# Performance work log

Hardware: AMD Instinct MI355X
Metric: run time of the kernel (lower is better)

Reference implementation:

```python
import jax, jax.numpy as jnp
import numpy as np

N_NODES = 50000
N_EDGES = 1600000
IN_DIM = 256
OUT_DIM = 32
N_HEADS = 4
ALPHA = 0.2


def setup_inputs() -> dict:
    key = jax.random.key(0)
    k1, k2, k3, k4 = jax.random.split(key, 4)
    h = jax.random.normal(k1, (N_NODES, IN_DIM), dtype=jnp.float32)
    adj_indices = jax.random.randint(k2, (2, N_EDGES), 0, N_NODES, dtype=jnp.int32)
    # xavier_uniform with gain=1.414 (matching torch init scale)
    def xavier(k, shape, gain=1.414):
        fan_in, fan_out = shape[0], shape[1]
        lim = gain * np.sqrt(6.0 / (fan_in + fan_out))
        return jax.random.uniform(k, shape, jnp.float32, -lim, lim)
    W = xavier(k3, (IN_DIM, OUT_DIM * N_HEADS))
    a = xavier(k4, (2 * OUT_DIM, N_HEADS))
    return {"h": h, "adj_indices": adj_indices, "W": W, "a": a}


def reference(h, adj_indices, W, a):
    N = h.shape[0]
    # project: [N, H, D]
    h_prime = (h @ W).reshape(N, N_HEADS, OUT_DIM)
    src = adj_indices[0]
    dst = adj_indices[1]
    h_src = h_prime[src]  # [E, H, D]
    h_dst = h_prime[dst]  # [E, H, D]
    a_src = a[:OUT_DIM]   # [D, H]
    a_dst = a[OUT_DIM:]   # [D, H]
    # attention logits per edge, per head: [E, H]
    att = jnp.einsum('ehd,dh->eh', h_src, a_src) + jnp.einsum('ehd,dh->eh', h_dst, a_dst)
    att = jax.nn.leaky_relu(att, negative_slope=ALPHA)
    # scatter-softmax over destination nodes (stable)
    m = jax.ops.segment_max(att, dst, num_segments=N)          # [N, H]
    e = jnp.exp(att - m[dst])                                   # [E, H]
    s = jax.ops.segment_sum(e, dst, num_segments=N)             # [N, H]
    att_norm = e / s[dst]                                       # [E, H]
    # weighted scatter-add aggregation: [N, H, D]
    agg = jax.ops.segment_sum(att_norm[:, :, None] * h_src, dst, num_segments=N)
    out = agg.reshape(N, N_HEADS * OUT_DIM)
    # dropout=0.0 (eval / identity)
    return out
```

## Files before the change

### kernel.cpp

```cpp
#include <hip/hip_runtime.h>

#define N_NODES 50000
#define N_EDGES 1600000
#define IN_DIM  256
#define OUT_D   128
#define NEG_SLOPE 0.2f
#define NBIN 256
#define BINW 196
#define CAP  8192
#define KDUP 8
#define NPW  25
#define SCAP 1536

typedef unsigned short ushort_t;
typedef short bf16x8 __attribute__((ext_vector_type(8)));
typedef float f32x4 __attribute__((ext_vector_type(4)));

__device__ __forceinline__ ushort_t f2bf(float f) {
    unsigned u = __float_as_uint(f);
    u = (u + 0x7FFF + ((u >> 16) & 1)) >> 16;
    return (ushort_t)u;
}

__global__ __launch_bounds__(256) void wprep_kernel(const float* __restrict__ W,
                                                    ushort_t* __restrict__ wt) {
    int i0 = (blockIdx.x * 256 + threadIdx.x) * 4;
    f32x4 v = *(const f32x4*)(W + i0);
    int k = i0 >> 7;
    int n0 = i0 & 127;
    int byte_in_row = 2 * k;
#pragma unroll
    for (int j = 0; j < 4; ++j) {
        int n = n0 + j;
        int sw = ((byte_in_row & ~15) ^ ((n & 7) << 4)) | (byte_in_row & 15);
        wt[(n << 8) + (sw >> 1)] = f2bf(v[j]);
    }
}

__global__ __launch_bounds__(256) void gemm_kernel(const float* __restrict__ h,
                                                   const ushort_t* __restrict__ wt,
                                                   const float* __restrict__ a,
                                                   ushort_t* __restrict__ hp,
                                                   float* __restrict__ asrc,
                                                   float* __restrict__ adst) {
    __shared__ ushort_t sW[32768];
    int t = threadIdx.x;
    for (int i = t * 8; i < 32768; i += 2048)
        *(bf16x8*)(sW + i) = *(const bf16x8*)(wt + i);
    __syncthreads();

    int wave = t >> 6, lane = t & 63;
    int l15 = lane & 15, quad = lane >> 4;
    int rowbase = blockIdx.x * 128 + wave * 16;

    f32x4 acc[2][8] = {};
#pragma unroll
    for (int ks = 0; ks < 8; ++ks) {
        bf16x8 af[2];
#pragma unroll
        for (int rt = 0; rt < 2; ++rt) {
            int arow = rowbase + rt * 64 + l15;
            if (arow >= N_NODES) arow = N_NODES - 1;
            const float* ap = h + (size_t)arow * IN_DIM + quad * 8 + ks * 32;
            f32x4 lo = *(const f32x4*)ap;
            f32x4 hi = *(const f32x4*)(ap + 4);
#pragma unroll
            for (int j = 0; j < 4; ++j) {
                af[rt][j]     = (short)f2bf(lo[j]);
                af[rt][4 + j] = (short)f2bf(hi[j]);
            }
        }
        int koff = ks * 64 + quad * 16;
#pragma unroll
        for (int tn = 0; tn < 8; ++tn) {
            int n = tn * 16 + l15;
            int swz = koff ^ ((n & 7) << 4);
            bf16x8 bfr = *(const bf16x8*)((const char*)sW + n * 512 + swz);
            acc[0][tn] = __builtin_amdgcn_mfma_f32_16x16x32_bf16(af[0], bfr, acc[0][tn], 0, 0, 0);
            acc[1][tn] = __builtin_amdgcn_mfma_f32_16x16x32_bf16(af[1], bfr, acc[1][tn], 0, 0, 0);
        }
    }

    float aS[8], aD[8];
#pragma unroll
    for (int tn = 0; tn < 8; ++tn) {
        int col = tn * 16 + l15;
        int dd = col & 31, hh = col >> 5;
        aS[tn] = a[dd * 4 + hh];
        aD[tn] = a[(32 + dd) * 4 + hh];
    }

#pragma unroll
    for (int rt = 0; rt < 2; ++rt)
#pragma unroll
        for (int r = 0; r < 4; ++r) {
            int row = rowbase + rt * 64 + quad * 4 + r;
            float pS[4] = {0.f, 0.f, 0.f, 0.f}, pD[4] = {0.f, 0.f, 0.f, 0.f};
#pragma unroll
            for (int tn = 0; tn < 8; ++tn) {
                float v = acc[rt][tn][r];
                pS[tn >> 1] += v * aS[tn];
                pD[tn >> 1] += v * aD[tn];
            }
#pragma unroll
            for (int o = 1; o < 16; o <<= 1) {
#pragma unroll
                for (int hh = 0; hh < 4; ++hh) {
                    pS[hh] += __shfl_xor(pS[hh], o, 16);
                    pD[hh] += __shfl_xor(pD[hh], o, 16);
                }
            }
            if (row < N_NODES) {
                if (l15 == 0) { f32x4 v = {pS[0], pS[1], pS[2], pS[3]}; *(f32x4*)(asrc + row * 4) = v; }
                if (l15 == 1) { f32x4 v = {pD[0], pD[1], pD[2], pD[3]}; *(f32x4*)(adst + row * 4) = v; }
            }
        }

#pragma unroll
    for (int rt = 0; rt < 2; ++rt)
#pragma unroll
        for (int tn = 0; tn < 8; ++tn) {
            int col = tn * 16 + l15;
#pragma unroll
            for (int r = 0; r < 4; ++r) {
                int row = rowbase + rt * 64 + quad * 4 + r;
                if (row < N_NODES) hp[(size_t)row * OUT_D + col] = f2bf(acc[rt][tn][r]);
            }
        }
}

__global__ __launch_bounds__(256) void binA_kernel(const int* __restrict__ src,
                                                   const int* __restrict__ dst,
                                                   int* __restrict__ tail,
                                                   unsigned* __restrict__ binbuf) {
    __shared__ unsigned stage[8192];
    __shared__ int cnt[256], lcnt[256], lbase[256], gbase[256], sc[256];
    int t = threadIdx.x;
    cnt[t] = 0; lcnt[t] = 0;
    __syncthreads();

    int blockbase = blockIdx.x * 8192;
    int n = min(8192, N_EDGES - blockbase);
    int e0 = blockbase + t * 32;
    int d[32], s[32];
#pragma unroll
    for (int q = 0; q < 8; ++q) {
        if (t * 32 + q * 4 + 4 <= n) {
            int4 dv = *(const int4*)(dst + e0 + q * 4);
            int4 sv = *(const int4*)(src + e0 + q * 4);
            d[q*4+0]=dv.x; d[q*4+1]=dv.y; d[q*4+2]=dv.z; d[q*4+3]=dv.w;
            s[q*4+0]=sv.x; s[q*4+1]=sv.y; s[q*4+2]=sv.z; s[q*4+3]=sv.w;
        } else {
#pragma unroll
            for (int r = 0; r < 4; ++r) {
                int g = t * 32 + q * 4 + r;
                d[q*4+r] = (g < n) ? dst[e0 + q*4 + r] : -1;
                s[q*4+r] = (g < n) ? src[e0 + q*4 + r] : 0;
            }
        }
    }
#pragma unroll
    for (int j = 0; j < 32; ++j)
        if (d[j] >= 0) atomicAdd(&cnt[(unsigned)d[j] / BINW], 1);
    __syncthreads();
    gbase[t] = atomicAdd(&tail[t], cnt[t]);
    sc[t] = cnt[t]; __syncthreads();
#pragma unroll
    for (int off = 1; off < 256; off <<= 1) {
        int v = (t >= off) ? sc[t - off] : 0;
        __syncthreads();
        sc[t] += v;
        __syncthreads();
    }
    lbase[t] = sc[t] - cnt[t];
    __syncthreads();
#pragma unroll
    for (int j = 0; j < 32; ++j) {
        if (d[j] >= 0) {
            unsigned p = (unsigned)d[j] / BINW;
            unsigned ldst = (unsigned)d[j] - p * BINW;
            int pos = lbase[p] + atomicAdd(&lcnt[p], 1);
            stage[pos] = (unsigned)s[j] | (ldst << 16) | (p << 24);
        }
    }
    __syncthreads();
    for (int i = t; i < n; i += 256) {
        unsigned v = stage[i];
        unsigned p = v >> 24;
        int pos = gbase[p] + (i - lbase[p]);
        if (pos < CAP) binbuf[(size_t)p * CAP + pos] = v & 0xFFFFFFu;
    }
}

__global__ __launch_bounds__(256) void aggB_kernel(const unsigned* __restrict__ binbuf,
                                                   const int* __restrict__ tail,
                                                   const float* __restrict__ asrc,
                                                   const float* __restrict__ adst,
                                                   const ushort_t* __restrict__ hp,
                                                   float* __restrict__ out) {
    int b = blockIdx.x >> 3, j = blockIdx.x & 7;
    __shared__ ushort_t lcsr[SCAP];
    __shared__ int cnt[32], sc[32], excl[32], lcur[32];
    __shared__ int   s_i[4][64];
    __shared__ f32x4 s_p[4][64];
    int t = threadIdx.x;
    int count = min(tail[b], CAP);
    const unsigned* buf = binbuf + (size_t)b * CAP;
    int lo = j * NPW;
    int hi = min(lo + NPW, BINW);

    if (t < 32) cnt[t] = 0;
    __syncthreads();
    for (int i = t; i < count; i += 256) {
        int ld = (buf[i] >> 16) & 0xFF;
        if (ld >= lo && ld < hi) atomicAdd(&cnt[ld - lo], 1);
    }
    __syncthreads();
    if (t < 64) {
        int v = (t < 32) ? cnt[t] : 0;
#pragma unroll
        for (int off = 1; off < 32; off <<= 1) {
            int u = __shfl_up(v, off, 64);
            if (t >= off) v += u;
        }
        if (t < 32) { sc[t] = v; excl[t] = v - cnt[t]; lcur[t] = v - cnt[t]; }
    }
    __syncthreads();
    for (int i = t; i < count; i += 256) {
        unsigned v = buf[i];
        int ld = (v >> 16) & 0xFF;
        if (ld >= lo && ld < hi) {
            int pos = atomicAdd(&lcur[ld - lo], 1);
            if (pos < SCAP) lcsr[pos] = (ushort_t)(v & 0xFFFF);
        }
    }
    __syncthreads();

    int wave = t >> 6, lane = t & 63;
    int l15 = lane & 15, grp = lane >> 4;
    int hd = l15 >> 2;

    for (int ld = lo + wave; ld < hi; ld += 4) {
        int d = b * BINW + ld;
        if (d >= N_NODES) continue;
        int s0 = min(excl[ld - lo], SCAP), s1 = min(sc[ld - lo], SCAP);
        f32x4 ad = *(const f32x4*)(adst + d * 4);
        float sum[4] = {0.f, 0.f, 0.f, 0.f};
        f32x4 accA = {0.f, 0.f, 0.f, 0.f}, accB = {0.f, 0.f, 0.f, 0.f};

        for (int base = s0; base < s1; base += 64) {
            int n = min(64, s1 - base);
            int e = base + lane;
            bool ok = e < s1;
            int s = ok ? (int)lcsr[e] : 0;
            f32x4 p4 = {0.f, 0.f, 0.f, 0.f};
            if (ok) {
                f32x4 as = *(const f32x4*)(asrc + s * 4);
#pragma unroll
                for (int hh = 0; hh < 4; ++hh) {
                    float v = as[hh] + ad[hh];
                    v = v > 0.f ? v : NEG_SLOPE * v;
                    v = fminf(v, 80.f);
                    float p = __expf(v);
                    p4[hh] = p;
                    sum[hh] += p;
                }
            }
            s_i[wave][lane] = s;
            s_p[wave][lane] = p4;
            __builtin_amdgcn_wave_barrier();
            int iters = (n + 3) >> 2;
#pragma unroll 2
            for (int it = 0; it < iters; ++it) {
                int ei = it * 4 + grp;
                int se = s_i[wave][ei];
                float w = s_p[wave][ei][hd];
                const char* rp = (const char*)hp + ((size_t)se << 8) + l15 * 16;
                uint4 u = *(const uint4*)rp;
                accA[0] += w * __uint_as_float(u.x << 16);
                accA[1] += w * __uint_as_float(u.x & 0xFFFF0000u);
                accA[2] += w * __uint_as_float(u.y << 16);
                accA[3] += w * __uint_as_float(u.y & 0xFFFF0000u);
                accB[0] += w * __uint_as_float(u.z << 16);
                accB[1] += w * __uint_as_float(u.z & 0xFFFF0000u);
                accB[2] += w * __uint_as_float(u.w << 16);
                accB[3] += w * __uint_as_float(u.w & 0xFFFF0000u);
            }
            __builtin_amdgcn_wave_barrier();
        }
#pragma unroll
        for (int o = 16; o < 64; o <<= 1) {
#pragma unroll
            for (int q = 0; q < 4; ++q) {
                accA[q] += __shfl_xor(accA[q], o, 64);
                accB[q] += __shfl_xor(accB[q], o, 64);
            }
        }
#pragma unroll
        for (int o = 1; o < 64; o <<= 1) {
#pragma unroll
            for (int hh = 0; hh < 4; ++hh) sum[hh] += __shfl_xor(sum[hh], o, 64);
        }
        if (grp == 0) {
            float den = sum[hd];
            float inv = (den > 0.f) ? 1.f / den : 0.f;
            f32x4 r0, r1;
#pragma unroll
            for (int q = 0; q < 4; ++q) { r0[q] = accA[q] * inv; r1[q] = accB[q] * inv; }
            float* op = out + (size_t)d * OUT_D + l15 * 8;
            *(f32x4*)op = r0;
            *(f32x4*)(op + 4) = r1;
        }
    }
}

extern "C" void kernel_launch(void* const* d_in, const int* in_sizes, int n_in,
                              void* d_out, int out_size, void* d_ws, size_t ws_size,
                              hipStream_t stream) {
    const float* h   = (const float*)d_in[0];
    const int*   adj = (const int*)d_in[1];
    const float* W   = (const float*)d_in[2];
    const float* a   = (const float*)d_in[3];
    float*       out = (float*)d_out;

    const int* src = adj;
    const int* dst = adj + N_EDGES;

    char* ws = (char*)d_ws;
    size_t o = 0;
    auto alloc = [&](size_t bytes) -> void* {
        void* p = ws + o;
        o = (o + bytes + 255) & ~(size_t)255;
        return p;
    };
    ushort_t* hp     = (ushort_t*)alloc((size_t)N_NODES * OUT_D * 2);
    ushort_t* wt     = (ushort_t*)alloc((size_t)32768 * 2);
    float*    asrc   = (float*)alloc((size_t)N_NODES * 4 * 4);
    float*    adstp  = (float*)alloc((size_t)N_NODES * 4 * 4);
    int*      tail   = (int*)alloc((size_t)NBIN * 4);
    unsigned* binbuf = (unsigned*)alloc((size_t)NBIN * CAP * 4);

    hipMemsetAsync(tail, 0, (size_t)NBIN * 4, stream);

    wprep_kernel<<<32, 256, 0, stream>>>(W, wt);
    gemm_kernel<<<(N_NODES + 127) / 128, 256, 0, stream>>>(h, wt, a, hp, asrc, adstp);
    binA_kernel<<<(N_EDGES + 8191) / 8192, 256, 0, stream>>>(src, dst, tail, binbuf);
    aggB_kernel<<<NBIN * KDUP, 256, 0, stream>>>(binbuf, tail, asrc, adstp, hp, out);
}
```

Baseline: 209.5 us.

## Use fine-grained 25-node bins so aggregation blocks read only their own edges

Destination binning moves from 256 bins of 196 nodes to 2048 slots of 25 nodes, and each aggregation block owns one bin. Before, each of 8 duplicate blocks re-scanned the whole 196-node bin and filtered it. This removes the redundant 8x scan of bin buffers and the filtering branches. binA now keeps 2048 shared counters with a two-level scan, and it does many more global tail atomics per block. CAP 1152 per bin, roughly 800 edges expected, may overflow and silently drop edges.

```diff
diff --git a/kernel.cpp b/kernel.cpp
--- a/kernel.cpp
+++ b/kernel.cpp
@@ -5,12 +5,10 @@
 #define IN_DIM  256
 #define OUT_D   128
 #define NEG_SLOPE 0.2f
-#define NBIN 256
-#define BINW 196
-#define CAP  8192
-#define KDUP 8
-#define NPW  25
-#define SCAP 1536
+#define NBIN 2048
+#define NBINA 2000
+#define BINW 25
+#define CAP  1152
 
 typedef unsigned short ushort_t;
 typedef short bf16x8 __attribute__((ext_vector_type(8)));
@@ -134,9 +132,10 @@
                                                    int* __restrict__ tail,
                                                    unsigned* __restrict__ binbuf) {
     __shared__ unsigned stage[8192];
-    __shared__ int cnt[256], lcnt[256], lbase[256], gbase[256], sc[256];
+    __shared__ int cnt[NBIN], lcnt[NBIN], lbase[NBIN], gbase[NBIN];
+    __shared__ int sc[256];
     int t = threadIdx.x;
-    cnt[t] = 0; lcnt[t] = 0;
+    for (int i = t; i < NBIN; i += 256) { cnt[i] = 0; lcnt[i] = 0; }
     __syncthreads();
 
     int blockbase = blockIdx.x * 8192;
@@ -163,8 +162,12 @@
     for (int j = 0; j < 32; ++j)
         if (d[j] >= 0) atomicAdd(&cnt[(unsigned)d[j] / BINW], 1);
     __syncthreads();
-    gbase[t] = atomicAdd(&tail[t], cnt[t]);
-    sc[t] = cnt[t]; __syncthreads();
+
+    int base = t * 8, run = 0, loc[8];
+#pragma unroll
+    for (int r = 0; r < 8; ++r) { loc[r] = run; run += cnt[base + r]; }
+    sc[t] = run;
+    __syncthreads();
 #pragma unroll
     for (int off = 1; off < 256; off <<= 1) {
         int v = (t >= off) ? sc[t - off] : 0;
@@ -172,23 +175,30 @@
         sc[t] += v;
         __syncthreads();
     }
-    lbase[t] = sc[t] - cnt[t];
-    __syncthreads();
+    int ex = sc[t] - run;
+#pragma unroll
+    for (int r = 0; r < 8; ++r) {
+        int bb = base + r;
+        lbase[bb] = ex + loc[r];
+        gbase[bb] = atomicAdd(&tail[bb], cnt[bb]);
+    }
+    __syncthreads();
+
 #pragma unroll
     for (int j = 0; j < 32; ++j) {
         if (d[j] >= 0) {
             unsigned p = (unsigned)d[j] / BINW;
             unsigned ldst = (unsigned)d[j] - p * BINW;
             int pos = lbase[p] + atomicAdd(&lcnt[p], 1);
-            stage[pos] = (unsigned)s[j] | (ldst << 16) | (p << 24);
+            stage[pos] = (unsigned)s[j] | (ldst << 16) | (p << 21);
         }
     }
     __syncthreads();
     for (int i = t; i < n; i += 256) {
         unsigned v = stage[i];
-        unsigned p = v >> 24;
+        unsigned p = v >> 21;
         int pos = gbase[p] + (i - lbase[p]);
-        if (pos < CAP) binbuf[(size_t)p * CAP + pos] = v & 0xFFFFFFu;
+        if (pos < CAP) binbuf[(size_t)p * CAP + pos] = v & 0x1FFFFFu;
     }
 }
 
@@ -198,23 +208,19 @@
                                                    const float* __restrict__ adst,
                                                    const ushort_t* __restrict__ hp,
                                                    float* __restrict__ out) {
-    int b = blockIdx.x >> 3, j = blockIdx.x & 7;
-    __shared__ ushort_t lcsr[SCAP];
+    int b = blockIdx.x;
+    __shared__ ushort_t lcsr[CAP];
     __shared__ int cnt[32], sc[32], excl[32], lcur[32];
     __shared__ int   s_i[4][64];
     __shared__ f32x4 s_p[4][64];
     int t = threadIdx.x;
     int count = min(tail[b], CAP);
     const unsigned* buf = binbuf + (size_t)b * CAP;
-    int lo = j * NPW;
-    int hi = min(lo + NPW, BINW);
 
     if (t < 32) cnt[t] = 0;
     __syncthreads();
-    for (int i = t; i < count; i += 256) {
-        int ld = (buf[i] >> 16) & 0xFF;
-        if (ld >= lo && ld < hi) atomicAdd(&cnt[ld - lo], 1);
-    }
+    for (int i = t; i < count; i += 256)
+        atomicAdd(&cnt[(buf[i] >> 16) & 31], 1);
     __syncthreads();
     if (t < 64) {
         int v = (t < 32) ? cnt[t] : 0;
@@ -228,11 +234,9 @@
     __syncthreads();
     for (int i = t; i < count; i += 256) {
         unsigned v = buf[i];
-        int ld = (v >> 16) & 0xFF;
-        if (ld >= lo && ld < hi) {
-            int pos = atomicAdd(&lcur[ld - lo], 1);
-            if (pos < SCAP) lcsr[pos] = (ushort_t)(v & 0xFFFF);
-        }
+        int ld = (v >> 16) & 31;
+        int pos = atomicAdd(&lcur[ld], 1);
+        lcsr[pos] = (ushort_t)(v & 0xFFFF);
     }
     __syncthreads();
 
@@ -240,10 +244,10 @@
     int l15 = lane & 15, grp = lane >> 4;
     int hd = l15 >> 2;
 
-    for (int ld = lo + wave; ld < hi; ld += 4) {
+    for (int ld = wave; ld < BINW; ld += 4) {
         int d = b * BINW + ld;
         if (d >= N_NODES) continue;
-        int s0 = min(excl[ld - lo], SCAP), s1 = min(sc[ld - lo], SCAP);
+        int s0 = excl[ld], s1 = sc[ld];
         f32x4 ad = *(const f32x4*)(adst + d * 4);
         float sum[4] = {0.f, 0.f, 0.f, 0.f};
         f32x4 accA = {0.f, 0.f, 0.f, 0.f}, accB = {0.f, 0.f, 0.f, 0.f};
@@ -345,5 +349,5 @@
     wprep_kernel<<<32, 256, 0, stream>>>(W, wt);
     gemm_kernel<<<(N_NODES + 127) / 128, 256, 0, stream>>>(h, wt, a, hp, asrc, adstp);
     binA_kernel<<<(N_EDGES + 8191) / 8192, 256, 0, stream>>>(src, dst, tail, binbuf);
-    aggB_kernel<<<NBIN * KDUP, 256, 0, stream>>>(binbuf, tail, asrc, adstp, hp, out);
-}
+    aggB_kernel<<<NBINA, 256, 0, stream>>>(binbuf, tail, asrc, adstp, hp, out);
+}
```

Measured after the change: 218.6 us. 4.3% more time.

## Fuse GEMM with edge binning and add a fine-binning pass before aggregation

Applied to the files above, without the earlier changes.

Merges the projection GEMM and the coarse edge-binning pass into one launch with disjoint block ranges, so the compute-bound and scatter-bound work can run concurrently. The GEMM now reads B fragments straight from global memory (unswizzled layout) instead of staging W in shared memory. A new pass sorts each coarse bin into 8 fine sub-bins, so each aggregation block reads only its own edges instead of rescanning the whole coarse bin twice. This adds a launch and a read-write of the bin buffer, and the capacity of each sub-bin (LCAP) is now a hard cutoff.

```diff
diff --git a/kernel.cpp b/kernel.cpp
--- a/kernel.cpp
+++ b/kernel.cpp
@@ -8,9 +8,11 @@
 #define NBIN 256
 #define BINW 196
 #define CAP  8192
-#define KDUP 8
-#define NPW  25
-#define SCAP 1536
+#define NFINE 8
+#define FBINW 25
+#define LCAP 1152
+#define GEMM_BLOCKS 391
+#define BINA_BLOCKS 196
 
 typedef unsigned short ushort_t;
 typedef short bf16x8 __attribute__((ext_vector_type(8)));
@@ -28,193 +30,251 @@
     f32x4 v = *(const f32x4*)(W + i0);
     int k = i0 >> 7;
     int n0 = i0 & 127;
-    int byte_in_row = 2 * k;
-#pragma unroll
-    for (int j = 0; j < 4; ++j) {
-        int n = n0 + j;
-        int sw = ((byte_in_row & ~15) ^ ((n & 7) << 4)) | (byte_in_row & 15);
-        wt[(n << 8) + (sw >> 1)] = f2bf(v[j]);
-    }
-}
-
-__global__ __launch_bounds__(256) void gemm_kernel(const float* __restrict__ h,
-                                                   const ushort_t* __restrict__ wt,
-                                                   const float* __restrict__ a,
-                                                   ushort_t* __restrict__ hp,
-                                                   float* __restrict__ asrc,
-                                                   float* __restrict__ adst) {
-    __shared__ ushort_t sW[32768];
+#pragma unroll
+    for (int j = 0; j < 4; ++j)
+        wt[((n0 + j) << 8) + k] = f2bf(v[j]);
+}
+
+__global__ __launch_bounds__(256, 4) void gemmbin_kernel(
+        const float* __restrict__ h, const ushort_t* __restrict__ wt,
+        const float* __restrict__ a,
+        const int* __restrict__ src, const int* __restrict__ dst,
+        ushort_t* __restrict__ hp, float* __restrict__ asrc,
+        float* __restrict__ adst,
+        int* __restrict__ tail, unsigned* __restrict__ binbuf) {
     int t = threadIdx.x;
-    for (int i = t * 8; i < 32768; i += 2048)
-        *(bf16x8*)(sW + i) = *(const bf16x8*)(wt + i);
-    __syncthreads();
-
-    int wave = t >> 6, lane = t & 63;
-    int l15 = lane & 15, quad = lane >> 4;
-    int rowbase = blockIdx.x * 128 + wave * 16;
-
-    f32x4 acc[2][8] = {};
-#pragma unroll
-    for (int ks = 0; ks < 8; ++ks) {
-        bf16x8 af[2];
-#pragma unroll
-        for (int rt = 0; rt < 2; ++rt) {
-            int arow = rowbase + rt * 64 + l15;
-            if (arow >= N_NODES) arow = N_NODES - 1;
-            const float* ap = h + (size_t)arow * IN_DIM + quad * 8 + ks * 32;
-            f32x4 lo = *(const f32x4*)ap;
-            f32x4 hi = *(const f32x4*)(ap + 4);
-#pragma unroll
-            for (int j = 0; j < 4; ++j) {
-                af[rt][j]     = (short)f2bf(lo[j]);
-                af[rt][4 + j] = (short)f2bf(hi[j]);
-            }
-        }
-        int koff = ks * 64 + quad * 16;
-#pragma unroll
-        for (int tn = 0; tn < 8; ++tn) {
-            int n = tn * 16 + l15;
-            int swz = koff ^ ((n & 7) << 4);
-            bf16x8 bfr = *(const bf16x8*)((const char*)sW + n * 512 + swz);
-            acc[0][tn] = __builtin_amdgcn_mfma_f32_16x16x32_bf16(af[0], bfr, acc[0][tn], 0, 0, 0);
-            acc[1][tn] = __builtin_amdgcn_mfma_f32_16x16x32_bf16(af[1], bfr, acc[1][tn], 0, 0, 0);
-        }
-    }
-
-    float aS[8], aD[8];
-#pragma unroll
-    for (int tn = 0; tn < 8; ++tn) {
-        int col = tn * 16 + l15;
-        int dd = col & 31, hh = col >> 5;
-        aS[tn] = a[dd * 4 + hh];
-        aD[tn] = a[(32 + dd) * 4 + hh];
-    }
-
-#pragma unroll
-    for (int rt = 0; rt < 2; ++rt)
-#pragma unroll
-        for (int r = 0; r < 4; ++r) {
-            int row = rowbase + rt * 64 + quad * 4 + r;
-            float pS[4] = {0.f, 0.f, 0.f, 0.f}, pD[4] = {0.f, 0.f, 0.f, 0.f};
+    if (blockIdx.x < GEMM_BLOCKS) {
+        int wave = t >> 6, lane = t & 63;
+        int l15 = lane & 15, quad = lane >> 4;
+        int rowbase = blockIdx.x * 128 + wave * 16;
+
+        f32x4 acc[2][8] = {};
+#pragma unroll
+        for (int ks = 0; ks < 8; ++ks) {
+            bf16x8 af[2];
+#pragma unroll
+            for (int rt = 0; rt < 2; ++rt) {
+                int arow = rowbase + rt * 64 + l15;
+                if (arow >= N_NODES) arow = N_NODES - 1;
+                const float* ap = h + (size_t)arow * IN_DIM + quad * 8 + ks * 32;
+                f32x4 lo = *(const f32x4*)ap;
+                f32x4 hi = *(const f32x4*)(ap + 4);
+#pragma unroll
+                for (int j = 0; j < 4; ++j) {
+                    af[rt][j]     = (short)f2bf(lo[j]);
+                    af[rt][4 + j] = (short)f2bf(hi[j]);
+                }
+            }
 #pragma unroll
             for (int tn = 0; tn < 8; ++tn) {
-                float v = acc[rt][tn][r];
-                pS[tn >> 1] += v * aS[tn];
-                pD[tn >> 1] += v * aD[tn];
-            }
-#pragma unroll
-            for (int o = 1; o < 16; o <<= 1) {
-#pragma unroll
-                for (int hh = 0; hh < 4; ++hh) {
-                    pS[hh] += __shfl_xor(pS[hh], o, 16);
-                    pD[hh] += __shfl_xor(pD[hh], o, 16);
-                }
-            }
-            if (row < N_NODES) {
-                if (l15 == 0) { f32x4 v = {pS[0], pS[1], pS[2], pS[3]}; *(f32x4*)(asrc + row * 4) = v; }
-                if (l15 == 1) { f32x4 v = {pD[0], pD[1], pD[2], pD[3]}; *(f32x4*)(adst + row * 4) = v; }
-            }
-        }
-
-#pragma unroll
-    for (int rt = 0; rt < 2; ++rt)
+                int n = tn * 16 + l15;
+                bf16x8 bfr = *(const bf16x8*)(wt + (n << 8) + ks * 32 + quad * 8);
+                acc[0][tn] = __builtin_amdgcn_mfma_f32_16x16x32_bf16(af[0], bfr, acc[0][tn], 0, 0, 0);
+                acc[1][tn] = __builtin_amdgcn_mfma_f32_16x16x32_bf16(af[1], bfr, acc[1][tn], 0, 0, 0);
+            }
+        }
+
+        float aS[8], aD[8];
 #pragma unroll
         for (int tn = 0; tn < 8; ++tn) {
             int col = tn * 16 + l15;
+            int dd = col & 31, hh = col >> 5;
+            aS[tn] = a[dd * 4 + hh];
+            aD[tn] = a[(32 + dd) * 4 + hh];
+        }
+
+#pragma unroll
+        for (int rt = 0; rt < 2; ++rt)
 #pragma unroll
             for (int r = 0; r < 4; ++r) {
                 int row = rowbase + rt * 64 + quad * 4 + r;
-                if (row < N_NODES) hp[(size_t)row * OUT_D + col] = f2bf(acc[rt][tn][r]);
-            }
-        }
-}
-
-__global__ __launch_bounds__(256) void binA_kernel(const int* __restrict__ src,
-                                                   const int* __restrict__ dst,
-                                                   int* __restrict__ tail,
-                                                   unsigned* __restrict__ binbuf) {
-    __shared__ unsigned stage[8192];
-    __shared__ int cnt[256], lcnt[256], lbase[256], gbase[256], sc[256];
-    int t = threadIdx.x;
-    cnt[t] = 0; lcnt[t] = 0;
-    __syncthreads();
-
-    int blockbase = blockIdx.x * 8192;
-    int n = min(8192, N_EDGES - blockbase);
-    int e0 = blockbase + t * 32;
-    int d[32], s[32];
-#pragma unroll
-    for (int q = 0; q < 8; ++q) {
-        if (t * 32 + q * 4 + 4 <= n) {
-            int4 dv = *(const int4*)(dst + e0 + q * 4);
-            int4 sv = *(const int4*)(src + e0 + q * 4);
-            d[q*4+0]=dv.x; d[q*4+1]=dv.y; d[q*4+2]=dv.z; d[q*4+3]=dv.w;
-            s[q*4+0]=sv.x; s[q*4+1]=sv.y; s[q*4+2]=sv.z; s[q*4+3]=sv.w;
-        } else {
-#pragma unroll
-            for (int r = 0; r < 4; ++r) {
-                int g = t * 32 + q * 4 + r;
-                d[q*4+r] = (g < n) ? dst[e0 + q*4 + r] : -1;
-                s[q*4+r] = (g < n) ? src[e0 + q*4 + r] : 0;
-            }
-        }
-    }
-#pragma unroll
-    for (int j = 0; j < 32; ++j)
-        if (d[j] >= 0) atomicAdd(&cnt[(unsigned)d[j] / BINW], 1);
-    __syncthreads();
-    gbase[t] = atomicAdd(&tail[t], cnt[t]);
-    sc[t] = cnt[t]; __syncthreads();
-#pragma unroll
-    for (int off = 1; off < 256; off <<= 1) {
-        int v = (t >= off) ? sc[t - off] : 0;
+                float pS[4] = {0.f, 0.f, 0.f, 0.f}, pD[4] = {0.f, 0.f, 0.f, 0.f};
+#pragma unroll
+                for (int tn = 0; tn < 8; ++tn) {
+                    float v = acc[rt][tn][r];
+                    pS[tn >> 1] += v * aS[tn];
+                    pD[tn >> 1] += v * aD[tn];
+                }
+#pragma unroll
+                for (int o = 1; o < 16; o <<= 1) {
+#pragma unroll
+                    for (int hh = 0; hh < 4; ++hh) {
+                        pS[hh] += __shfl_xor(pS[hh], o, 16);
+                        pD[hh] += __shfl_xor(pD[hh], o, 16);
+                    }
+                }
+                if (row < N_NODES) {
+                    if (l15 == 0) { f32x4 v = {pS[0], pS[1], pS[2], pS[3]}; *(f32x4*)(asrc + row * 4) = v; }
+                    if (l15 == 1) { f32x4 v = {pD[0], pD[1], pD[2], pD[3]}; *(f32x4*)(adst + row * 4) = v; }
+                }
+            }
+
+#pragma unroll
+        for (int rt = 0; rt < 2; ++rt)
+#pragma unroll
+            for (int tn = 0; tn < 8; ++tn) {
+                int col = tn * 16 + l15;
+#pragma unroll
+                for (int r = 0; r < 4; ++r) {
+                    int row = rowbase + rt * 64 + quad * 4 + r;
+                    if (row < N_NODES) hp[(size_t)row * OUT_D + col] = f2bf(acc[rt][tn][r]);
+                }
+            }
+    } else {
+        __shared__ unsigned stage[8192];
+        __shared__ int cnt[256], lcnt[256], lbase[256], gbase[256], sc[256];
+        int bid = blockIdx.x - GEMM_BLOCKS;
+        cnt[t] = 0; lcnt[t] = 0;
         __syncthreads();
-        sc[t] += v;
+
+        int blockbase = bid * 8192;
+        int n = min(8192, N_EDGES - blockbase);
+        int e0 = blockbase + t * 32;
+        int d[32], s[32];
+#pragma unroll
+        for (int q = 0; q < 8; ++q) {
+            if (t * 32 + q * 4 + 4 <= n) {
+                int4 dv = *(const int4*)(dst + e0 + q * 4);
+                int4 sv = *(const int4*)(src + e0 + q * 4);
+                d[q*4+0]=dv.x; d[q*4+1]=dv.y; d[q*4+2]=dv.z; d[q*4+3]=dv.w;
+                s[q*4+0]=sv.x; s[q*4+1]=sv.y; s[q*4+2]=sv.z; s[q*4+3]=sv.w;
+            } else {
+#pragma unroll
+                for (int r = 0; r < 4; ++r) {
+                    int g = t * 32 + q * 4 + r;
+                    d[q*4+r] = (g < n) ? dst[e0 + q*4 + r] : -1;
+                    s[q*4+r] = (g < n) ? src[e0 + q*4 + r] : 0;
+                }
+            }
+        }
+#pragma unroll
+        for (int j = 0; j < 32; ++j)
+            if (d[j] >= 0) atomicAdd(&cnt[(unsigned)d[j] / BINW], 1);
         __syncthreads();
-    }
-    lbase[t] = sc[t] - cnt[t];
-    __syncthreads();
-#pragma unroll
-    for (int j = 0; j < 32; ++j) {
-        if (d[j] >= 0) {
-            unsigned p = (unsigned)d[j] / BINW;
-            unsigned ldst = (unsigned)d[j] - p * BINW;
-            int pos = lbase[p] + atomicAdd(&lcnt[p], 1);
-            stage[pos] = (unsigned)s[j] | (ldst << 16) | (p << 24);
-        }
-    }
-    __syncthreads();
-    for (int i = t; i < n; i += 256) {
-        unsigned v = stage[i];
-        unsigned p = v >> 24;
-        int pos = gbase[p] + (i - lbase[p]);
-        if (pos < CAP) binbuf[(size_t)p * CAP + pos] = v & 0xFFFFFFu;
-    }
+        gbase[t] = atomicAdd(&tail[t], cnt[t]);
+        sc[t] = cnt[t]; __syncthreads();
+#pragma unroll
+        for (int off = 1; off < 256; off <<= 1) {
+            int v = (t >= off) ? sc[t - off] : 0;
+            __syncthreads();
+            sc[t] += v;
+            __syncthreads();
+        }
+        lbase[t] = sc[t] - cnt[t];
+        __syncthreads();
+#pragma unroll
+        for (int j = 0; j < 32; ++j) {
+            if (d[j] >= 0) {
+                unsigned p = (unsigned)d[j] / BINW;
+                unsigned ldst = (unsigned)d[j] - p * BINW;
+                int pos = lbase[p] + atomicAdd(&lcnt[p], 1);
+                stage[pos] = (unsigned)s[j] | (ldst << 16) | (p << 24);
+            }
+        }
+        __syncthreads();
+        for (int i = t; i < n; i += 256) {
+            unsigned v = stage[i];
+            unsigned p = v >> 24;
+            int pos = gbase[p] + (i - lbase[p]);
+            if (pos < CAP) binbuf[(size_t)p * CAP + pos] = v & 0xFFFFFFu;
+        }
+    }
+}
+
+__global__ __launch_bounds__(256) void binB_kernel(const int* __restrict__ tail,
+                                                   unsigned* __restrict__ binbuf,
+                                                   int* __restrict__ fbase,
+                                                   int* __restrict__ fcnt) {
+    int b = blockIdx.x, t = threadIdx.x;
+    __shared__ unsigned stg[CAP];
+    __shared__ int wtot[4][NFINE];
+    __shared__ int jbase[NFINE];
+    int wave = t >> 6, lane = t & 63;
+    int count = min(tail[b], CAP);
+    unsigned* buf = binbuf + (size_t)b * CAP;
+
+    int chunk = (count + 255) >> 8;
+    int lo = min(t * chunk, count), hi = min(lo + chunk, count);
+
+    int c[NFINE] = {0, 0, 0, 0, 0, 0, 0, 0};
+    for (int i = lo; i < hi; ++i) {
+        int j = (int)(buf[i] >> 16) / FBINW;
+#pragma unroll
+        for (int jj = 0; jj < NFINE; ++jj) c[jj] += (j == jj) ? 1 : 0;
+    }
+    int myb[NFINE];
+#pragma unroll
+    for (int jj = 0; jj < NFINE; ++jj) {
+        int v = c[jj];
+#pragma unroll
+        for (int off = 1; off < 64; off <<= 1) {
+            int u = __shfl_up(v, off, 64);
+            if (lane >= off) v += u;
+        }
+        myb[jj] = v - c[jj];
+        if (lane == 63) wtot[wave][jj] = v;
+    }
+    __syncthreads();
+    if (t == 0) {
+        int runj[NFINE];
+#pragma unroll
+        for (int jj = 0; jj < NFINE; ++jj) {
+            int r = 0;
+#pragma unroll
+            for (int w = 0; w < 4; ++w) { int x = wtot[w][jj]; wtot[w][jj] = r; r += x; }
+            runj[jj] = r;
+        }
+        int r = 0;
+#pragma unroll
+        for (int jj = 0; jj < NFINE; ++jj) {
+            jbase[jj] = r;
+            fbase[b * NFINE + jj] = r;
+            fcnt [b * NFINE + jj] = runj[jj];
+            r += runj[jj];
+        }
+    }
+    __syncthreads();
+    int pos[NFINE];
+#pragma unroll
+    for (int jj = 0; jj < NFINE; ++jj) pos[jj] = jbase[jj] + wtot[wave][jj] + myb[jj];
+    for (int i = lo; i < hi; ++i) {
+        unsigned v = buf[i];
+        int ldst = (int)(v >> 16);
+        int j = ldst / FBINW;
+        int p = 0;
+#pragma unroll
+        for (int jj = 0; jj < NFINE; ++jj) p = (j == jj) ? pos[jj] : p;
+        stg[p] = (v & 0xFFFFu) | ((unsigned)(ldst - j * FBINW) << 16);
+#pragma unroll
+        for (int jj = 0; jj < NFINE; ++jj) pos[jj] += (j == jj) ? 1 : 0;
+    }
+    __syncthreads();
+    for (int i = t; i < count; i += 256) buf[i] = stg[i];
 }
 
 __global__ __launch_bounds__(256) void aggB_kernel(const unsigned* __restrict__ binbuf,
-                                                   const int* __restrict__ tail,
+                                                   const int* __restrict__ fbase,
+                                                   const int* __restrict__ fcnt,
                                                    const float* __restrict__ asrc,
                                                    const float* __restrict__ adst,
                                                    const ushort_t* __restrict__ hp,
                                                    float* __restrict__ out) {
-    int b = blockIdx.x >> 3, j = blockIdx.x & 7;
-    __shared__ ushort_t lcsr[SCAP];
+    int bid = blockIdx.x;
+    int b = bid >> 3, fj = bid & 7;
+    __shared__ ushort_t lcsr[LCAP];
     __shared__ int cnt[32], sc[32], excl[32], lcur[32];
     __shared__ int   s_i[4][64];
     __shared__ f32x4 s_p[4][64];
     int t = threadIdx.x;
-    int count = min(tail[b], CAP);
-    const unsigned* buf = binbuf + (size_t)b * CAP;
-    int lo = j * NPW;
-    int hi = min(lo + NPW, BINW);
+    int count = min(fcnt[bid], LCAP);
+    const unsigned* buf = binbuf + (size_t)b * CAP + fbase[bid];
+    int dbase = b * BINW + fj * FBINW;
+    int nd = min(FBINW, BINW - fj * FBINW);
 
     if (t < 32) cnt[t] = 0;
     __syncthreads();
-    for (int i = t; i < count; i += 256) {
-        int ld = (buf[i] >> 16) & 0xFF;
-        if (ld >= lo && ld < hi) atomicAdd(&cnt[ld - lo], 1);
-    }
+    for (int i = t; i < count; i += 256)
+        atomicAdd(&cnt[(buf[i] >> 16) & 31], 1);
     __syncthreads();
     if (t < 64) {
         int v = (t < 32) ? cnt[t] : 0;
@@ -228,11 +288,9 @@
     __syncthreads();
     for (int i = t; i < count; i += 256) {
         unsigned v = buf[i];
-        int ld = (v >> 16) & 0xFF;
-        if (ld >= lo && ld < hi) {
-            int pos = atomicAdd(&lcur[ld - lo], 1);
-            if (pos < SCAP) lcsr[pos] = (ushort_t)(v & 0xFFFF);
-        }
+        int ld = (v >> 16) & 31;
+        int pos = atomicAdd(&lcur[ld], 1);
+        lcsr[pos] = (ushort_t)(v & 0xFFFF);
     }
     __syncthreads();
 
@@ -240,10 +298,10 @@
     int l15 = lane & 15, grp = lane >> 4;
     int hd = l15 >> 2;
 
-    for (int ld = lo + wave; ld < hi; ld += 4) {
-        int d = b * BINW + ld;
+    for (int ld = wave; ld < nd; ld += 4) {
+        int d = dbase + ld;
         if (d >= N_NODES) continue;
-        int s0 = min(excl[ld - lo], SCAP), s1 = min(sc[ld - lo], SCAP);
+        int s0 = excl[ld], s1 = sc[ld];
         f32x4 ad = *(const f32x4*)(adst + d * 4);
         float sum[4] = {0.f, 0.f, 0.f, 0.f};
         f32x4 accA = {0.f, 0.f, 0.f, 0.f}, accB = {0.f, 0.f, 0.f, 0.f};
@@ -339,11 +397,14 @@
     float*    adstp  = (float*)alloc((size_t)N_NODES * 4 * 4);
     int*      tail   = (int*)alloc((size_t)NBIN * 4);
     unsigned* binbuf = (unsigned*)alloc((size_t)NBIN * CAP * 4);
+    int*      fbase  = (int*)alloc((size_t)NBIN * NFINE * 4);
+    int*      fcnt   = (int*)alloc((size_t)NBIN * NFINE * 4);
 
     hipMemsetAsync(tail, 0, (size_t)NBIN * 4, stream);
 
     wprep_kernel<<<32, 256, 0, stream>>>(W, wt);
-    gemm_kernel<<<(N_NODES + 127) / 128, 256, 0, stream>>>(h, wt, a, hp, asrc, adstp);
-    binA_kernel<<<(N_EDGES + 8191) / 8192, 256, 0, stream>>>(src, dst, tail, binbuf);
-    aggB_kernel<<<NBIN * KDUP, 256, 0, stream>>>(binbuf, tail, asrc, adstp, hp, out);
-}
+    gemmbin_kernel<<<GEMM_BLOCKS + BINA_BLOCKS, 256, 0, stream>>>(
+        h, wt, a, src, dst, hp, asrc, adstp, tail, binbuf);
+    binB_kernel<<<NBIN, 256, 0, stream>>>(tail, binbuf, fbase, fcnt);
+    aggB_kernel<<<NBIN * NFINE, 256, 0, stream>>>(binbuf, fbase, fcnt, asrc, adstp, hp, out);
+}
```

New measurement: 203.8 us. 1.03x faster.
